# Kernel optimization log

Hardware: AMD Instinct MI355X
Metric: run time of the kernel (lower is better)

The kernel has to match this reference:

```python
import jax, jax.numpy as jnp
import numpy as np

D = 128  # hard-coded hidden dim in MLP_T

def setup_inputs() -> dict:
    key = jax.random.key(0)
    ks = jax.random.split(key, 8)
    N, IN = 16384, 768
    return {
        "x": jax.random.normal(ks[0], (N, IN), dtype=jnp.float32),
        "decay_value": 1,
        "W_token": jax.random.normal(ks[1], (IN, D), dtype=jnp.float32) * (IN ** -0.5),
        "b_token": jax.random.normal(ks[2], (D,), dtype=jnp.float32) * 0.02,
        "W_qkv": jax.random.normal(ks[3], (D, 3 * D), dtype=jnp.float32) * (D ** -0.5),
        "b_qkv": jax.random.normal(ks[4], (3 * D,), dtype=jnp.float32) * 0.02,
        "W_fc": jax.random.normal(ks[5], (D, 1), dtype=jnp.float32) * (D ** -0.5),
        "b_fc": jax.random.normal(ks[6], (1,), dtype=jnp.float32) * 0.02,
    }

def reference(x, decay_value, W_token, b_token, W_qkv, b_qkv, W_fc, b_fc):
    # token projection: [N, in_chan] -> [N, 128]
    h = x @ W_token + b_token
    # qkv: [N, 384] split along feature dim into q, k, v of [N, 128]
    qkv = h @ W_qkv + b_qkv
    q, k, v = qkv[:, :D], qkv[:, D:2 * D], qkv[:, 2 * D:]
    # sigmoid attention (no row normalization); dropout is identity in eval mode
    att_scores = jax.nn.sigmoid(q @ k.T)            # [N, N]
    att = att_scores @ v                            # [N, 128]
    out = att @ W_fc + b_fc                         # [N, 1]
    # GradientReversal is identity in the forward pass
    return out
```

## Files before the change

### kernel.cpp

```cpp
#include <hip/hip_runtime.h>
#include <hip/hip_bf16.h>
#include <stdint.h>

#define N_ROWS 16384

typedef __bf16 bf16x8 __attribute__((ext_vector_type(8)));
typedef float f32x4 __attribute__((ext_vector_type(4)));

#define AS1 __attribute__((address_space(1)))
#define AS3 __attribute__((address_space(3)))

#define OFF_WCS  0u
#define OFF_BC   589824u
#define OFF_QB   591360u
#define OFF_KB   4785664u
#define OFF_WV   8979968u
#define OFF_PART 9045504u

__global__ void prep(const float* __restrict__ Wt, const float* __restrict__ Wq,
                     const float* __restrict__ bt, const float* __restrict__ bq,
                     __bf16* __restrict__ WcS, float* __restrict__ bc) {
    int u = blockIdx.x * 256 + threadIdx.x;
    if (u < 768 * 96) {
        int k = u / 96, n4 = u % 96;
        float s[4] = {0, 0, 0, 0};
        const float* wtp = Wt + k * 128;
        const float* wqp = Wq + n4 * 4;
#pragma unroll 8
        for (int d = 0; d < 128; d++) {
            float a = wtp[d];
            float4 b = *(const float4*)(wqp + d * 384);
            s[0] += a * b.x; s[1] += a * b.y; s[2] += a * b.z; s[3] += a * b.w;
        }
        int kb_ = k >> 6, c = (k >> 3) & 7, k7 = k & 7;
#pragma unroll
        for (int j = 0; j < 4; j++) {
            int n = n4 * 4 + j;
            WcS[n * 768 + kb_ * 64 + ((c ^ (n & 7)) << 3) + k7] = (__bf16)s[j];
        }
    }
    if (u < 384) {
        float s = bq[u];
        for (int d = 0; d < 128; d++) s += bt[d] * Wq[d * 384 + u];
        bc[u] = s;
    }
}

__launch_bounds__(256)
__global__ void gemm_qkv(const float* __restrict__ x, const __bf16* __restrict__ WcS,
                         const float* __restrict__ bc, const float* __restrict__ W_fc,
                         __bf16* __restrict__ qb, __bf16* __restrict__ kb,
                         float* __restrict__ wv) {
    __shared__ float  Asm[64 * 64];
    __shared__ __bf16 Bsm[128 * 64];
    __shared__ float  wred[64];
    const int tid = threadIdx.x, wave = tid >> 6, lane = tid & 63;
    const int n16 = lane & 15, q = lane >> 4;
    const int mh = wave >> 1, nw = wave & 1;
    const int row0 = blockIdx.x * 64;
    const int sp = blockIdx.y;

    const char* aptr[4];
    const char* bptr[4];
    {
        int p = (lane & 15) >> 1, half = lane & 1;
#pragma unroll
        for (int i = 0; i < 4; i++) {
            int ar = row0 + wave * 16 + i * 4 + (lane >> 4);
            aptr[i] = (const char*)x + (size_t)ar * 3072 + ((p ^ (ar & 7)) * 8 + half * 4) * 4;
            int br = sp * 128 + wave * 32 + i * 8 + (lane >> 3);
            bptr[i] = (const char*)WcS + (size_t)br * 1536 + (lane & 7) * 16;
        }
    }
    f32x4 acc[2][4];
#pragma unroll
    for (int mt = 0; mt < 2; mt++)
#pragma unroll
        for (int t = 0; t < 4; t++) acc[mt][t] = (f32x4){0, 0, 0, 0};

    for (int kbi = 0; kbi < 12; kbi++) {
#pragma unroll
        for (int i = 0; i < 4; i++)
            __builtin_amdgcn_global_load_lds((const AS1 void*)(aptr[i] + kbi * 256),
                (AS3 void*)((char*)Asm + wave * 4096 + i * 1024), 16, 0, 0);
#pragma unroll
        for (int i = 0; i < 4; i++)
            __builtin_amdgcn_global_load_lds((const AS1 void*)(bptr[i] + kbi * 128),
                (AS3 void*)((char*)Bsm + wave * 4096 + i * 1024), 16, 0, 0);
        __syncthreads();
#pragma unroll
        for (int ks = 0; ks < 2; ks++) {
            const int swz = ((ks * 4 + q) ^ (n16 & 7)) << 3;
            bf16x8 af[2];
#pragma unroll
            for (int mt = 0; mt < 2; mt++) {
                const float* ap = Asm + (mh * 32 + mt * 16 + n16) * 64 + swz;
                f32x4 a0 = *(const f32x4*)ap;
                f32x4 a1 = *(const f32x4*)(ap + 4);
                bf16x8 t;
                t[0] = (__bf16)a0[0]; t[1] = (__bf16)a0[1]; t[2] = (__bf16)a0[2]; t[3] = (__bf16)a0[3];
                t[4] = (__bf16)a1[0]; t[5] = (__bf16)a1[1]; t[6] = (__bf16)a1[2]; t[7] = (__bf16)a1[3];
                af[mt] = t;
            }
#pragma unroll
            for (int t = 0; t < 4; t++) {
                bf16x8 bf = *(const bf16x8*)(Bsm + (nw * 64 + t * 16 + n16) * 64 + swz);
                acc[0][t] = __builtin_amdgcn_mfma_f32_16x16x32_bf16(af[0], bf, acc[0][t], 0, 0, 0);
                acc[1][t] = __builtin_amdgcn_mfma_f32_16x16x32_bf16(af[1], bf, acc[1][t], 0, 0, 0);
            }
        }
        __syncthreads();
    }

    const int clb = nw * 64 + n16;
    if (sp == 0) {
#pragma unroll
        for (int t = 0; t < 4; t++) {
            int cl = clb + t * 16;
            float bcv = bc[cl];
#pragma unroll
            for (int mt = 0; mt < 2; mt++)
#pragma unroll
                for (int r = 0; r < 4; r++) {
                    int row = row0 + mh * 32 + mt * 16 + q * 4 + r;
                    qb[row * 128 + cl] = (__bf16)((acc[mt][t][r] + bcv) * -1.44269504088896f);
                }
        }
    } else if (sp == 1) {
#pragma unroll
        for (int t = 0; t < 4; t++) {
            int d = clb + t * 16;
            float bcv = bc[128 + d];
#pragma unroll
            for (int mt = 0; mt < 2; mt++)
#pragma unroll
                for (int r = 0; r < 4; r++) {
                    int row = row0 + mh * 32 + mt * 16 + q * 4 + r;
                    kb[row * 128 + (((d >> 3) ^ (row & 15)) << 3) + (d & 7)] = (__bf16)(acc[mt][t][r] + bcv);
                }
        }
    } else {
        float wacc[2][4] = {{0, 0, 0, 0}, {0, 0, 0, 0}};
#pragma unroll
        for (int t = 0; t < 4; t++) {
            int cl = clb + t * 16;
            float bcv = bc[256 + cl];
            float wf = W_fc[cl];
#pragma unroll
            for (int mt = 0; mt < 2; mt++)
#pragma unroll
                for (int r = 0; r < 4; r++) wacc[mt][r] += (acc[mt][t][r] + bcv) * wf;
        }
        float vred[2][4];
#pragma unroll
        for (int mt = 0; mt < 2; mt++)
#pragma unroll
            for (int r = 0; r < 4; r++) {
                float v = wacc[mt][r];
                v += __shfl_xor(v, 1, 64);
                v += __shfl_xor(v, 2, 64);
                v += __shfl_xor(v, 4, 64);
                v += __shfl_xor(v, 8, 64);
                vred[mt][r] = v;
                if (nw == 0 && n16 == 0) wred[mh * 32 + mt * 16 + q * 4 + r] = v;
            }
        __syncthreads();
        if (nw == 1 && n16 == 0) {
#pragma unroll
            for (int mt = 0; mt < 2; mt++)
#pragma unroll
                for (int r = 0; r < 4; r++) {
                    int lr = mh * 32 + mt * 16 + q * 4 + r;
                    wv[row0 + lr] = wred[lr] + vred[mt][r];
                }
        }
    }
}

__launch_bounds__(128, 4)
__global__ void attn(const __bf16* __restrict__ qb, const __bf16* __restrict__ kb,
                     const float* __restrict__ wv, float* __restrict__ partial) {
    __shared__ __bf16 kbuf[64 * 128];
    __shared__ float wbuf[64];
    const int tid = threadIdx.x;
    const int wave = tid >> 6, lane = tid & 63;
    const int n16 = lane & 15, q = lane >> 4;
    const int row0 = blockIdx.x * 64 + wave * 32;
    const int sp = blockIdx.y;
    bf16x8 qf[2][4];
#pragma unroll
    for (int mt = 0; mt < 2; mt++)
#pragma unroll
        for (int ks = 0; ks < 4; ks++)
            qf[mt][ks] = *(const bf16x8*)(qb + (row0 + mt * 16 + n16) * 128 + ks * 32 + q * 8);
    float acc[2][4] = {{0}, {0}};
    for (int jc = 0; jc < 32; jc++) {
        const int jbase = sp * 2048 + jc * 64;
        const char* gsrc = (const char*)kb + (size_t)jbase * 256;
#pragma unroll
        for (int i = 0; i < 8; i++) {
            const int off = wave * 8192 + i * 1024;
            __builtin_amdgcn_global_load_lds(
                (const AS1 void*)(gsrc + off + lane * 16),
                (AS3 void*)((char*)kbuf + off), 16, 0, 0);
        }
        if (tid < 64) wbuf[tid] = wv[jbase + tid];
        __syncthreads();
#pragma unroll
        for (int t = 0; t < 4; t++) {
            f32x4 s[2];
#pragma unroll
            for (int mt = 0; mt < 2; mt++) s[mt] = (f32x4){0, 0, 0, 0};
#pragma unroll
            for (int ks = 0; ks < 4; ks++) {
                const int chunk = (ks * 4 + q) ^ n16;
                bf16x8 bf = *(const bf16x8*)(kbuf + (t * 16 + n16) * 128 + chunk * 8);
                s[0] = __builtin_amdgcn_mfma_f32_16x16x32_bf16(qf[0][ks], bf, s[0], 0, 0, 0);
                s[1] = __builtin_amdgcn_mfma_f32_16x16x32_bf16(qf[1][ks], bf, s[1], 0, 0, 0);
            }
            const float wval = wbuf[t * 16 + n16];
#pragma unroll
            for (int mt = 0; mt < 2; mt++)
#pragma unroll
                for (int r = 0; r < 4; r++)
                    acc[mt][r] += __builtin_amdgcn_rcpf(1.0f + __builtin_amdgcn_exp2f(s[mt][r])) * wval;
        }
        __syncthreads();
    }
#pragma unroll
    for (int mt = 0; mt < 2; mt++)
#pragma unroll
        for (int r = 0; r < 4; r++) {
            float v = acc[mt][r];
            v += __shfl_xor(v, 1, 64);
            v += __shfl_xor(v, 2, 64);
            v += __shfl_xor(v, 4, 64);
            v += __shfl_xor(v, 8, 64);
            if (n16 == 0) partial[sp * N_ROWS + row0 + mt * 16 + q * 4 + r] = v;
        }
}

__global__ void reduce_out(const float* __restrict__ partial, const float* __restrict__ b_fc,
                           float* __restrict__ out) {
    int i = blockIdx.x * 256 + threadIdx.x;
    float v = b_fc[0];
#pragma unroll
    for (int s = 0; s < 8; s++) v += partial[s * N_ROWS + i];
    out[i] = v;
}

extern "C" void kernel_launch(void* const* d_in, const int* in_sizes, int n_in,
                              void* d_out, int out_size, void* d_ws, size_t ws_size,
                              hipStream_t stream) {
    const float* x       = (const float*)d_in[0];
    const float* W_token = (const float*)d_in[2];
    const float* b_token = (const float*)d_in[3];
    const float* W_qkv   = (const float*)d_in[4];
    const float* b_qkv   = (const float*)d_in[5];
    const float* W_fc    = (const float*)d_in[6];
    const float* b_fc    = (const float*)d_in[7];
    float* out = (float*)d_out;
    char* ws = (char*)d_ws;

    __bf16* WcS = (__bf16*)(ws + OFF_WCS);
    float*  bc  = (float*)(ws + OFF_BC);
    __bf16* qb  = (__bf16*)(ws + OFF_QB);
    __bf16* kb  = (__bf16*)(ws + OFF_KB);
    float*  wv  = (float*)(ws + OFF_WV);
    float*  part = (float*)(ws + OFF_PART);

    prep<<<288, 256, 0, stream>>>(W_token, W_qkv, b_token, b_qkv, WcS, bc);
    gemm_qkv<<<dim3(256, 3), 256, 0, stream>>>(x, WcS, bc, W_fc, qb, kb, wv);
    attn<<<dim3(256, 8), 128, 0, stream>>>(qb, kb, wv, part);
    reduce_out<<<64, 256, 0, stream>>>(part, b_fc, out);
}
```

Measured before the change: 213.3 us.

## Double-buffer K tiles in LDS to overlap loads with MFMA compute

The attention kernel moves from single-buffered 64-key chunks with two barriers per iteration to double-buffered 32-key chunks. The global-to-LDS loads for the next chunk are issued before computing on the current one, with one barrier per iteration. The aim is to hide global load latency behind MFMA and sigmoid work. In exchange it runs twice as many iterations with smaller tiles and does one redundant reload at the last step. It also relies on the async LDS writes finishing by the single barrier.

```diff
diff --git a/kernel.cpp b/kernel.cpp
--- a/kernel.cpp
+++ b/kernel.cpp
@@ -180,13 +180,15 @@
 __launch_bounds__(128, 4)
 __global__ void attn(const __bf16* __restrict__ qb, const __bf16* __restrict__ kb,
                      const float* __restrict__ wv, float* __restrict__ partial) {
-    __shared__ __bf16 kbuf[64 * 128];
-    __shared__ float wbuf[64];
+    __shared__ __bf16 kbuf[2 * 32 * 128];
+    __shared__ float wbuf[2 * 32];
     const int tid = threadIdx.x;
     const int wave = tid >> 6, lane = tid & 63;
     const int n16 = lane & 15, q = lane >> 4;
     const int row0 = blockIdx.x * 64 + wave * 32;
     const int sp = blockIdx.y;
+    const int jb0 = sp * 2048;
+
     bf16x8 qf[2][4];
 #pragma unroll
     for (int mt = 0; mt < 2; mt++)
@@ -194,39 +196,60 @@
         for (int ks = 0; ks < 4; ks++)
             qf[mt][ks] = *(const bf16x8*)(qb + (row0 + mt * 16 + n16) * 128 + ks * 32 + q * 8);
     float acc[2][4] = {{0}, {0}};
-    for (int jc = 0; jc < 32; jc++) {
-        const int jbase = sp * 2048 + jc * 64;
-        const char* gsrc = (const char*)kb + (size_t)jbase * 256;
-#pragma unroll
-        for (int i = 0; i < 8; i++) {
-            const int off = wave * 8192 + i * 1024;
-            __builtin_amdgcn_global_load_lds(
-                (const AS1 void*)(gsrc + off + lane * 16),
-                (AS3 void*)((char*)kbuf + off), 16, 0, 0);
-        }
-        if (tid < 64) wbuf[tid] = wv[jbase + tid];
-        __syncthreads();
-#pragma unroll
-        for (int t = 0; t < 4; t++) {
-            f32x4 s[2];
-#pragma unroll
-            for (int mt = 0; mt < 2; mt++) s[mt] = (f32x4){0, 0, 0, 0};
+
+    {
+        const char* gsrc = (const char*)kb + (size_t)jb0 * 256;
+        float w0 = wv[jb0 + (tid & 31)];
+#pragma unroll
+        for (int i = 0; i < 4; i++) {
+            const int off = wave * 4096 + i * 1024;
+            __builtin_amdgcn_global_load_lds((const AS1 void*)(gsrc + off + lane * 16),
+                                             (AS3 void*)((char*)kbuf + off), 16, 0, 0);
+        }
+        if (tid < 32) wbuf[tid] = w0;
+        __syncthreads();
+    }
+
+#pragma unroll 2
+    for (int jc = 0; jc < 64; jc++) {
+        const int cb = jc & 1;
+        const __bf16* curK = kbuf + cb * (32 * 128);
+        __bf16* nxtK = kbuf + (cb ^ 1) * (32 * 128);
+        const float* curW = wbuf + cb * 32;
+        float* nxtW = wbuf + (cb ^ 1) * 32;
+        const int jn = (jc + 1 < 64) ? jc + 1 : 63;
+
+        float wnext = wv[jb0 + jn * 32 + (tid & 31)];
+        const char* gsrc = (const char*)kb + (size_t)(jb0 + jn * 32) * 256;
+#pragma unroll
+        for (int i = 0; i < 4; i++) {
+            const int off = wave * 4096 + i * 1024;
+            __builtin_amdgcn_global_load_lds((const AS1 void*)(gsrc + off + lane * 16),
+                                             (AS3 void*)((char*)nxtK + off), 16, 0, 0);
+        }
+
+#pragma unroll
+        for (int t = 0; t < 2; t++) {
+            f32x4 s0 = (f32x4){0, 0, 0, 0}, s1 = (f32x4){0, 0, 0, 0};
 #pragma unroll
             for (int ks = 0; ks < 4; ks++) {
                 const int chunk = (ks * 4 + q) ^ n16;
-                bf16x8 bf = *(const bf16x8*)(kbuf + (t * 16 + n16) * 128 + chunk * 8);
-                s[0] = __builtin_amdgcn_mfma_f32_16x16x32_bf16(qf[0][ks], bf, s[0], 0, 0, 0);
-                s[1] = __builtin_amdgcn_mfma_f32_16x16x32_bf16(qf[1][ks], bf, s[1], 0, 0, 0);
-            }
-            const float wval = wbuf[t * 16 + n16];
-#pragma unroll
-            for (int mt = 0; mt < 2; mt++)
-#pragma unroll
-                for (int r = 0; r < 4; r++)
-                    acc[mt][r] += __builtin_amdgcn_rcpf(1.0f + __builtin_amdgcn_exp2f(s[mt][r])) * wval;
-        }
-        __syncthreads();
-    }
+                bf16x8 bf = *(const bf16x8*)(curK + (t * 16 + n16) * 128 + chunk * 8);
+                s0 = __builtin_amdgcn_mfma_f32_16x16x32_bf16(qf[0][ks], bf, s0, 0, 0, 0);
+                s1 = __builtin_amdgcn_mfma_f32_16x16x32_bf16(qf[1][ks], bf, s1, 0, 0, 0);
+            }
+            const float wval = curW[t * 16 + n16];
+#pragma unroll
+            for (int r = 0; r < 4; r++) {
+                acc[0][r] += __builtin_amdgcn_rcpf(1.0f + __builtin_amdgcn_exp2f(s0[r])) * wval;
+                acc[1][r] += __builtin_amdgcn_rcpf(1.0f + __builtin_amdgcn_exp2f(s1[r])) * wval;
+            }
+        }
+
+        if (tid < 32) nxtW[tid] = wnext;
+        __syncthreads();
+    }
+
 #pragma unroll
     for (int mt = 0; mt < 2; mt++)
 #pragma unroll
```

After: 218.9 us. 2.7% more time.
